# Performance work log

Measured on AMD Instinct MI355X. Metric: run time of the kernel, lower is better.

## Reference

```python
import jax, jax.numpy as jnp
import numpy as np

EPS = 1e-4
GX, GY, ZMAX = 512, 512, 64
S0 = (GX, GY, ZMAX)

# ---------- rulebook construction (numpy, setup-time only) ----------

def _lin(c, S):
    return (c[:, 0].astype(np.int64) * S[1] + c[:, 1]) * S[2] + c[:, 2]

def _lookup(skeys, order, qk):
    pos = np.searchsorted(skeys, qk)
    pc = np.clip(pos, 0, len(skeys) - 1)
    ok = skeys[pc] == qk
    return np.where(ok, order[pc], -1).astype(np.int32)

def _sm_rulebook(coords, S):
    # submanifold 3x3x3: for each active site, index of neighbor at each of 27 offsets (-1 if inactive)
    keys = _lin(coords, S)
    order = np.argsort(keys).astype(np.int64); skeys = keys[order]
    Sa = np.array(S)
    cols = []
    for d in [(i, j, k) for i in (-1, 0, 1) for j in (-1, 0, 1) for k in (-1, 0, 1)]:
        q = coords + np.array(d)
        inb = np.all((q >= 0) & (q < Sa), axis=1)
        nb = _lookup(skeys, order, _lin(np.clip(q, 0, None), S))
        cols.append(np.where(inb, nb, -1).astype(np.int32))
    return np.stack(cols, 1)  # [N, 27]

def _down_rulebook(coords, S):
    # strided 2x2x2 conv: coarse sites = unique(coords//2); [Nc, 8] child indices into fine level
    Sc = (S[0] // 2, S[1] // 2, S[2] // 2)
    pk = np.unique(_lin(coords // 2, Sc))
    z = pk % Sc[2]; y = (pk // Sc[2]) % Sc[1]; x = pk // (Sc[1] * Sc[2])
    pcoords = np.stack([x, y, z], 1)
    keys = _lin(coords, S)
    order = np.argsort(keys).astype(np.int64); skeys = keys[order]
    cols = []
    for d in [(i, j, k) for i in (0, 1) for j in (0, 1) for k in (0, 1)]:
        cols.append(_lookup(skeys, order, _lin(pcoords * 2 + np.array(d), S)))
    return np.stack(cols, 1), pcoords, Sc

def _coords0():
    # road-like 2.5D surface: one active voxel per (x, y) column -> exactly 512*512 unique sites
    xs, ys = np.meshgrid(np.arange(GX), np.arange(GY), indexing='ij')
    x = xs.ravel().astype(np.int64); y = ys.ravel().astype(np.int64)
    z = (32 + 8 * np.sin(x / 37.0) + 8 * np.cos(y / 53.0) + 3 * np.sin((x + y) / 17.0)).astype(np.int64)
    z = np.clip(z, 0, ZMAX - 1)
    return np.stack([x, y, z], 1)


def setup_inputs() -> dict:
    c0 = _coords0()
    nbr_0 = _sm_rulebook(c0, S0)
    rb_0, c1, S1 = _down_rulebook(c0, S0)
    nbr_1 = _sm_rulebook(c1, S1)
    rb_1, c2, S2 = _down_rulebook(c1, S1)
    nbr_2 = _sm_rulebook(c2, S2)

    key = jax.random.key(0)
    ks = iter(jax.random.split(key, 40))
    def w(shape):
        fan = float(np.prod(shape[:-1]))
        return (jax.random.normal(next(ks), shape, jnp.float32) / np.sqrt(fan)).astype(jnp.float32)
    def gb(c):  # row 0 = gamma (~1), row 1 = beta (~0)
        base = jnp.concatenate([jnp.ones((1, c), jnp.float32), jnp.zeros((1, c), jnp.float32)], 0)
        return base + 0.01 * jax.random.normal(next(ks), (2, c), jnp.float32)

    N0 = c0.shape[0]
    return dict(
        feat=jax.random.normal(next(ks), (N0, 3), jnp.float32),
        w_in=w((27, 3, 32)),
        bn1_0=gb(32), w_sm1_0=w((27, 32, 32)),
        bnd_0=gb(32), w_down_0=w((8, 32, 64)),
        bn1_1=gb(64), w_sm1_1=w((27, 64, 64)),
        bnd_1=gb(64), w_down_1=w((8, 64, 96)),
        bn1_2=gb(96), w_sm1_2=w((27, 96, 96)),
        bnu_1=gb(96), w_up_1=w((8, 96, 64)),
        bn2_1=gb(128), w_sm2_1=w((27, 128, 64)),
        bnu_0=gb(64), w_up_0=w((8, 64, 32)),
        bn2_0=gb(64), w_sm2_0=w((27, 64, 32)),
        bnf=gb(32),
        lin_w=w((32, 2)), lin_b=jnp.zeros((2,), jnp.float32),
        nbr_0=jnp.asarray(nbr_0), nbr_1=jnp.asarray(nbr_1), nbr_2=jnp.asarray(nbr_2),
        rb_0=jnp.asarray(rb_0), rb_1=jnp.asarray(rb_1),
    )

# ---------- jax forward ----------

def bn_relu(x, gb):
    # SCN BatchNormReLU: normalize over all active sites (biased var), affine, then ReLU
    mu = jnp.mean(x, 0)
    var = jnp.var(x, 0)
    return jax.nn.relu((x - mu) * (gb[0] / jnp.sqrt(var + EPS)) + gb[1])

def sm_conv(feat, nbr, W):
    # submanifold conv: gather 27 neighbors (zero for inactive), per-offset GEMM, accumulate
    out = jnp.zeros((feat.shape[0], W.shape[2]), feat.dtype)
    for k in range(W.shape[0]):
        idx = nbr[:, k]
        g = jnp.where((idx >= 0)[:, None], feat[jnp.clip(idx, 0)], 0.0)
        out = out + g @ W[k]
    return out

def down_conv(feat, rb, W):
    # strided 2x2x2 conv: gather children of each coarse site
    out = jnp.zeros((rb.shape[0], W.shape[2]), feat.dtype)
    for k in range(W.shape[0]):
        idx = rb[:, k]
        g = jnp.where((idx >= 0)[:, None], feat[jnp.clip(idx, 0)], 0.0)
        out = out + g @ W[k]
    return out

def up_conv(feat_c, rb, W, n_fine):
    # deconv (transpose of down_conv): scatter coarse features back to fine active sites
    out = jnp.zeros((n_fine, W.shape[2]), feat_c.dtype)
    for k in range(W.shape[0]):
        idx = rb[:, k]
        contrib = jnp.where((idx >= 0)[:, None], feat_c @ W[k], 0.0)
        out = out.at[jnp.clip(idx, 0)].add(contrib)
    return out


def reference(feat, w_in, bn1_0, w_sm1_0, bnd_0, w_down_0, bn1_1, w_sm1_1, bnd_1, w_down_1,
              bn1_2, w_sm1_2, bnu_1, w_up_1, bn2_1, w_sm2_1, bnu_0, w_up_0, bn2_0, w_sm2_0,
              bnf, lin_w, lin_b, nbr_0, nbr_1, nbr_2, rb_0, rb_1):
    x0 = sm_conv(feat, nbr_0, w_in)                              # initial SMConv 3 -> 32
    x0 = sm_conv(bn_relu(x0, bn1_0), nbr_0, w_sm1_0)             # level-0 entry block
    d0 = down_conv(bn_relu(x0, bnd_0), rb_0, w_down_0)           # [N1, 64]
    x1 = sm_conv(bn_relu(d0, bn1_1), nbr_1, w_sm1_1)             # level-1 entry block
    d1 = down_conv(bn_relu(x1, bnd_1), rb_1, w_down_1)           # [N2, 96]
    x2 = sm_conv(bn_relu(d1, bn1_2), nbr_2, w_sm1_2)             # innermost block
    u1 = up_conv(bn_relu(x2, bnu_1), rb_1, w_up_1, x1.shape[0])  # deconv 96 -> 64
    y1 = sm_conv(bn_relu(jnp.concatenate([x1, u1], 1), bn2_1), nbr_1, w_sm2_1)  # 128 -> 64
    u0 = up_conv(bn_relu(y1, bnu_0), rb_0, w_up_0, x0.shape[0])  # deconv 64 -> 32
    y0 = sm_conv(bn_relu(jnp.concatenate([x0, u0], 1), bn2_0), nbr_0, w_sm2_0)  # 64 -> 32
    out = bn_relu(y0, bnf)                                       # final BatchNormReLU(m)
    return out @ lin_w + lin_b                                   # Linear(m, 2)
```

## Files before the change

### kernel.cpp

```cpp
#include <hip/hip_runtime.h>
#include <hip/hip_bf16.h>


typedef __hip_bfloat16 hbf;
typedef __attribute__((ext_vector_type(8))) short short8;
typedef __attribute__((ext_vector_type(4))) float f32x4;
typedef const __attribute__((address_space(1))) short gas_short;
typedef __attribute__((address_space(3))) short las_short;

__device__ inline float b2f(short s) {
    unsigned u = ((unsigned)(unsigned short)s) << 16;
    float f; __builtin_memcpy(&f, &u, 4); return f;
}
__device__ inline short f2b(float f) {
    hbf h = __float2bfloat16(f);
    short s; __builtin_memcpy(&s, &h, 2); return s;
}

struct WPA {
    const float* src[9];
    short* dst[9];
    int CI[9], CO[9];
    int cum[10];
};
__global__ __launch_bounds__(256) void wprep_all(WPA a, int total) {
    int e0 = blockIdx.x * 256 + threadIdx.x;
    if (e0 >= total) return;
    int L = 0;
#pragma unroll
    for (int i = 1; i < 9; i++) L += (e0 >= a.cum[i]) ? 1 : 0;
    int e = e0 - a.cum[L];
    int CI = a.CI[L], CO = a.CO[L];
    int NT = CO >> 4, NCH = CI >> 5;
    int j    = e & 7;
    int lane = (e >> 3) & 63;
    int t    = (e >> 9) % NT;
    int c    = (e / (512 * NT)) % NCH;
    int k    = e / (512 * NT * NCH);
    int ci = c * 32 + (lane >> 4) * 8 + j;
    int co = t * 16 + (lane & 15);
    a.dst[L][e] = f2b(a.src[L][((long long)k * CI + ci) * CO + co]);
}

__global__ void zerok(float* p, int n) {
    int i = blockIdx.x * 256 + threadIdx.x;
    if (i < n) p[i] = 0.f;
}

__global__ __launch_bounds__(256) void nbrmask_k(const int* __restrict__ nbr,
                                                 unsigned* __restrict__ msk, int N) {
    long long r = (long long)blockIdx.x * 256 + threadIdx.x;
    if (r >= N) return;
    unsigned mv = 0;
#pragma unroll
    for (int k = 0; k < 27; k++)
        mv |= (nbr[r * 27 + k] >= 0) ? (1u << k) : 0u;
    msk[r] = mv;
}

__global__ __launch_bounds__(256) void conv_in_st(
    const float* __restrict__ feat, const unsigned* __restrict__ msk,
    const float* __restrict__ W, short* __restrict__ out, int N) {
    __shared__ float sW[27 * 96];
    __shared__ float sF[3][258][3];
    const int tid = threadIdx.x;
    const int bid = blockIdx.x;
    const int xq     = bid >> 1;
    const int ystart = (bid & 1) << 8;
    const long long R = (long long)bid * 256;

    for (int e = tid; e < 27 * 96; e += 256) sW[e] = W[e];
    for (int e = tid; e < 3 * 258; e += 256) {
        int rr = e % 258, st = e / 258;
        long long gr = (long long)(xq - 1 + st) * 512 + (ystart - 1 + rr);
        long long grc = (gr < 0 || gr >= N) ? 0 : gr;
        sF[st][rr][0] = feat[grc * 3];
        sF[st][rr][1] = feat[grc * 3 + 1];
        sF[st][rr][2] = feat[grc * 3 + 2];
    }
    __syncthreads();

    long long r = R + tid;
    unsigned mv = (r < N) ? msk[r] : 0u;
    float acc[32];
#pragma unroll
    for (int c = 0; c < 32; c++) acc[c] = 0.f;
#pragma unroll
    for (int k = 0; k < 27; k++) {
        if (mv & (1u << k)) {
            const int st = k / 9;
            const int dy = (k / 3) % 3 - 1;
            const int rl = 1 + tid + dy;
            float f0 = sF[st][rl][0];
            float f1 = sF[st][rl][1];
            float f2 = sF[st][rl][2];
            const float* w = sW + k * 96;
#pragma unroll
            for (int c = 0; c < 32; c++)
                acc[c] += f0 * w[c] + f1 * w[32 + c] + f2 * w[64 + c];
        }
    }
    if (r < N) {
#pragma unroll
        for (int c = 0; c < 32; c++) out[r * 32 + c] = f2b(acc[c]);
    }
}

template<int CI1, int CI2, int COUT>
__global__ __launch_bounds__(256) void stencil0(
    const short* __restrict__ fA, const short* __restrict__ fB,
    const unsigned* __restrict__ msk, const short* __restrict__ Wf,
    short* __restrict__ out, float* __restrict__ pstat,
    const float* __restrict__ abA, const float* __restrict__ abB, int N) {
    constexpr int CIT  = CI1 + CI2;
    constexpr int NCH  = CIT / 32;
    constexpr int NT   = COUT / 16;
    constexpr int MT   = 2;
    constexpr int CIB  = CIT * 2;
    constexpr int ROWS = 130;
    constexpr int NC8  = CIT / 8;
    constexpr int SWB  = (CIB >= 128) ? 7 : 3;
    __shared__ __attribute__((aligned(16))) char sA[3 * ROWS * CIB];
    const int tid  = threadIdx.x;
    const int lane = tid & 63;
    const int wid  = tid >> 6;
    const int m    = lane & 15;
    const int quad = lane >> 4;
    const int bid  = blockIdx.x;
    const int xq     = bid >> 2;
    const int ystart = (bid & 3) << 7;
    const long long R = (long long)bid * 128;

    {
        const int c8 = tid % NC8;
        const bool isA = (c8 * 8) < CI1;
        const short* src  = isA ? fA : fB;
        const float* abp  = isA ? abA : abB;
        const int   srcCI = isA ? CI1 : CI2;
        const int   chb   = isA ? c8 * 8 : c8 * 8 - CI1;
        float s_[8], b_[8];
#pragma unroll
        for (int jj = 0; jj < 8; jj++) {
            s_[jj] = abp[chb + jj];
            b_[jj] = abp[srcCI + chb + jj];
        }
        for (int e = tid; e < 3 * ROWS * NC8; e += 256) {
            int rr = (e / NC8) % ROWS;
            int st = e / (NC8 * ROWS);
            long long gr = (long long)(xq - 1 + st) * 512 + (ystart - 1 + rr);
            long long grc = (gr < 0 || gr >= N) ? 0 : gr;
            short8 v = *reinterpret_cast<const short8*>(src + grc * srcCI + chb);
            short8 o;
#pragma unroll
            for (int jj = 0; jj < 8; jj++) {
                float f = b2f(v[jj]) * s_[jj] + b_[jj];
                o[jj] = f2b(f > 0.f ? f : 0.f);
            }
            int byte = (st * ROWS + rr) * CIB + c8 * 16;
            byte ^= ((rr & SWB) << 4);
            *reinterpret_cast<short8*>(sA + byte) = o;
        }
    }
    __syncthreads();

    f32x4 acc[MT][NT];
#pragma unroll
    for (int mt = 0; mt < MT; mt++)
#pragma unroll
        for (int t = 0; t < NT; t++) acc[mt][t] = (f32x4)0.f;

    unsigned mv[MT];
#pragma unroll
    for (int mt = 0; mt < MT; mt++) {
        long long r = R + wid * 32 + mt * 16 + m;
        mv[mt] = (r < N) ? msk[r] : 0u;
    }

#pragma unroll
    for (int s9 = 0; s9 < 9; s9++) {
        const int st = s9 / 3;
        const int dy = s9 % 3 - 1;
        short8 a[MT][NCH];
#pragma unroll
        for (int mt = 0; mt < MT; mt++) {
            int rl = 1 + wid * 32 + mt * 16 + m + dy;
#pragma unroll
            for (int c = 0; c < NCH; c++) {
                int byte = (st * ROWS + rl) * CIB + (c * 4 + quad) * 16;
                byte ^= ((rl & SWB) << 4);
                a[mt][c] = *reinterpret_cast<const short8*>(sA + byte);
            }
        }
#pragma unroll
        for (int z3 = 0; z3 < 3; z3++) {
            const int k = s9 * 3 + z3;
            unsigned anyb = (mv[0] >> k) & 1;
            if (MT > 1) anyb |= (mv[1] >> k) & 1;
            if (__any(anyb)) {
                short8 bf[NCH][NT];
#pragma unroll
                for (int c = 0; c < NCH; c++)
#pragma unroll
                    for (int t = 0; t < NT; t++)
                        bf[c][t] = *reinterpret_cast<const short8*>(
                            Wf + ((size_t)(k * NCH + c) * NT + t) * 512 + lane * 8);
#pragma unroll
                for (int mt = 0; mt < MT; mt++) {
                    const bool bb = (mv[mt] >> k) & 1;
                    short8 asel[NCH];
#pragma unroll
                    for (int c = 0; c < NCH; c++)
                        asel[c] = bb ? a[mt][c] : (short8)0;
#pragma unroll
                    for (int c = 0; c < NCH; c++)
#pragma unroll
                        for (int t = 0; t < NT; t++)
                            acc[mt][t] = __builtin_amdgcn_mfma_f32_16x16x32_bf16(
                                asel[c], bf[c][t], acc[mt][t], 0, 0, 0);
                }
            }
        }
    }

    float s[NT], q[NT];
#pragma unroll
    for (int t = 0; t < NT; t++) { s[t] = 0.f; q[t] = 0.f; }
#pragma unroll
    for (int mt = 0; mt < MT; mt++) {
#pragma unroll
        for (int g4 = 0; g4 < 4; g4++) {
            long long sr = R + wid * 32 + mt * 16 + quad * 4 + g4;
            if (sr < N) {
#pragma unroll
                for (int t = 0; t < NT; t++) {
                    float v = acc[mt][t][g4];
                    out[sr * COUT + t * 16 + m] = f2b(v);
                    s[t] += v; q[t] += v * v;
                }
            }
        }
    }
    float* pb = pstat + (blockIdx.x & 7) * 2 * COUT;
#pragma unroll
    for (int t = 0; t < NT; t++) {
        float sv = s[t], qv = q[t];
        sv += __shfl_xor(sv, 16); qv += __shfl_xor(qv, 16);
        sv += __shfl_xor(sv, 32); qv += __shfl_xor(qv, 32);
        if (quad == 0) {
            atomicAdd(&pb[t * 16 + m], sv);
            atomicAdd(&pb[COUT + t * 16 + m], qv);
        }
    }
}

template<int CI1, int CI2, int COUT, int K, int G, int MT, bool FACT>
__global__ __launch_bounds__(256) void gmfma10(
    const short* __restrict__ fA, const short* __restrict__ fB,
    const int* __restrict__ nbr, const short* __restrict__ Wf,
    short* __restrict__ out, float* __restrict__ pstat,
    const float* __restrict__ abp, int N) {
    static_assert(K % G == 0, "G must divide K");
    static_assert(!FACT || CI2 == 0, "fused act only for single input");
    constexpr int NT  = COUT / 16;
    constexpr int NC1 = CI1 / 32;
    constexpr int NC2 = CI2 / 32;
    constexpr int NCH = (CI1 + CI2) / 32;
    constexpr int PANEL = NCH * NT * 512;
    constexpr int GSH   = G * PANEL;
    constexpr int NPH   = K / G;
    constexpr int WCH   = GSH / 4;
    constexpr int S16   = (WCH * 2) / 1024;
    constexpr int S4    = ((WCH * 2) % 1024) / 256;
    __shared__ __attribute__((aligned(16))) short sB[GSH];
    const int tid  = threadIdx.x;
    const int lane = tid & 63;
    const int wid  = tid >> 6;
    const int m    = lane & 15;
    const int quad = lane >> 4;
    const long long tb0 = ((long long)blockIdx.x * 4 + wid) * (MT * 16);

    f32x4 acc[MT][NT];
#pragma unroll
    for (int mt = 0; mt < MT; mt++)
#pragma unroll
        for (int t = 0; t < NT; t++) acc[mt][t] = (f32x4)0.f;

#define STAGE(ph)                                                              \
    {                                                                          \
        const short* _src = Wf + (size_t)(ph) * GSH + wid * WCH;               \
        short* _dst = &sB[wid * WCH];                                          \
        _Pragma("unroll")                                                      \
        for (int i = 0; i < S16; i++)                                          \
            __builtin_amdgcn_global_load_lds(                                  \
                (gas_short*)(_src + i * 512 + lane * 8),                       \
                (las_short*)(_dst + i * 512), 16, 0, 0);                       \
        _Pragma("unroll")                                                      \
        for (int i = 0; i < S4; i++)                                           \
            __builtin_amdgcn_global_load_lds(                                  \
                (gas_short*)(_src + S16 * 512 + i * 128 + lane * 2),           \
                (las_short*)(_dst + S16 * 512 + i * 128), 4, 0, 0);            \
    }

    STAGE(0)
    __builtin_amdgcn_sched_barrier(0);

    int idxs[MT][K];
#pragma unroll
    for (int mt = 0; mt < MT; mt++) {
        long long r = tb0 + mt * 16 + m;
        bool rv = r < N;
#pragma unroll
        for (int k = 0; k < K; k++)
            idxs[mt][k] = rv ? nbr[r * K + k] : -1;
    }
    unsigned pmask[MT];
#pragma unroll
    for (int mt = 0; mt < MT; mt++) {
        unsigned pm = 0;
#pragma unroll
        for (int k = 0; k < K; k++)
            pm |= __any(idxs[mt][k] >= 0) ? (1u << k) : 0u;
        pmask[mt] = __builtin_amdgcn_readfirstlane(pm);
    }

    float aS[FACT ? NC1 * 8 : 1], aBb[FACT ? NC1 * 8 : 1];
    if constexpr (FACT) {
#pragma unroll
        for (int c = 0; c < NC1; c++)
#pragma unroll
            for (int jj = 0; jj < 8; jj++) {
                int ch = c * 32 + quad * 8 + jj;
                aS[c * 8 + jj]  = abp[ch];
                aBb[c * 8 + jj] = abp[CI1 + ch];
            }
    }

    __builtin_amdgcn_sched_barrier(0);
    asm volatile("s_waitcnt vmcnt(0)" ::: "memory");
    __builtin_amdgcn_s_barrier();
    __builtin_amdgcn_sched_barrier(0);
    asm volatile("" ::: "memory");

    short8 S[3][NCH];

#define LOADS(sl, mt, kk)                                                      \
    {                                                                          \
        int _i = idxs[mt][kk];                                                 \
        long long _j = _i < 0 ? 0 : _i;                                        \
        _Pragma("unroll")                                                      \
        for (int c = 0; c < NC1; c++) {                                        \
            short8 _v = *reinterpret_cast<const short8*>(                      \
                fA + _j * CI1 + c * 32 + quad * 8);                            \
            if constexpr (FACT) {                                              \
                short8 _o;                                                     \
                _Pragma("unroll")                                              \
                for (int jj = 0; jj < 8; jj++) {                               \
                    float _f = b2f(_v[jj]) * aS[c * 8 + jj] + aBb[c * 8 + jj]; \
                    _o[jj] = f2b(_f > 0.f ? _f : 0.f);                         \
                }                                                              \
                _v = _o;                                                       \
            }                                                                  \
            S[sl][c] = (_i >= 0) ? _v : (short8)0;                             \
        }                                                                      \
        if constexpr (NC2 > 0) {                                               \
            _Pragma("unroll")                                                  \
            for (int c = 0; c < NC2; c++) {                                    \
                short8 _v = *reinterpret_cast<const short8*>(                  \
                    fB + _j * CI2 + c * 32 + quad * 8);                        \
                S[sl][NC1 + c] = (_i >= 0) ? _v : (short8)0;                   \
            }                                                                  \
        }                                                                      \
    }
#define MFMAS(sl, mt, jl)                                                      \
    {                                                                          \
        _Pragma("unroll")                                                      \
        for (int c = 0; c < NCH; c++) {                                        \
            _Pragma("unroll")                                                  \
            for (int t = 0; t < NT; t++) {                                     \
                short8 b = *reinterpret_cast<const short8*>(                   \
                    &sB[((jl) * NCH * NT + c * NT + t) * 512 + lane * 8]);     \
                acc[mt][t] = __builtin_amdgcn_mfma_f32_16x16x32_bf16(          \
                    S[sl][c], b, acc[mt][t], 0, 0, 0);                         \
            }                                                                  \
        }                                                                      \
    }

#pragma unroll
    for (int ph = 0; ph < NPH; ph++) {
#pragma unroll
        for (int mt = 0; mt < MT; mt++) {
            const unsigned mm = (pmask[mt] >> (ph * G)) & ((1u << G) - 1);
#pragma unroll
            for (int j = 0; j < G + 2; j++) {
                if (j < G)
                    if (mm & (1u << j)) LOADS(j % 3, mt, ph * G + j)
                if (j >= 2)
                    if (mm & (1u << (j - 2))) MFMAS((j - 2) % 3, mt, j - 2)
            }
        }
        if (ph + 1 < NPH) {
            __builtin_amdgcn_sched_barrier(0);
            asm volatile("s_waitcnt lgkmcnt(0)" ::: "memory");
            __builtin_amdgcn_s_barrier();
            __builtin_amdgcn_sched_barrier(0);
            STAGE(ph + 1)
            __builtin_amdgcn_sched_barrier(0);
            asm volatile("s_waitcnt vmcnt(0)" ::: "memory");
            __builtin_amdgcn_s_barrier();
            __builtin_amdgcn_sched_barrier(0);
            asm volatile("" ::: "memory");
        }
    }
#undef LOADS
#undef MFMAS
#undef STAGE
    float s[NT], q[NT];
#pragma unroll
    for (int t = 0; t < NT; t++) { s[t] = 0.f; q[t] = 0.f; }
#pragma unroll
    for (int mt = 0; mt < MT; mt++) {
#pragma unroll
        for (int g4 = 0; g4 < 4; g4++) {
            long long sr = tb0 + mt * 16 + quad * 4 + g4;
            if (sr < N) {
#pragma unroll
                for (int t = 0; t < NT; t++) {
                    float v = acc[mt][t][g4];
                    out[sr * COUT + t * 16 + m] = f2b(v);
                    s[t] += v; q[t] += v * v;
                }
            }
        }
    }
    float* pb = pstat + (blockIdx.x & 7) * 2 * COUT;
#pragma unroll
    for (int t = 0; t < NT; t++) {
        float sv = s[t], qv = q[t];
        sv += __shfl_xor(sv, 16); qv += __shfl_xor(qv, 16);
        sv += __shfl_xor(sv, 32); qv += __shfl_xor(qv, 32);
        if (quad == 0) {
            atomicAdd(&pb[t * 16 + m], sv);
            atomicAdd(&pb[COUT + t * 16 + m], qv);
        }
    }
}

template<int CIN, int COUT, int G>
__global__ __launch_bounds__(256) void upmfma10(
    const short* __restrict__ f, const int* __restrict__ rb,
    const short* __restrict__ Wf, short* __restrict__ out,
    float* __restrict__ pstat, const float* __restrict__ abp, int N) {
    static_assert(8 % G == 0, "G must divide 8");
    constexpr int NT = COUT / 16;
    constexpr int NK = CIN / 32;
    constexpr int PANEL = NK * NT * 512;
    constexpr int GSH   = G * PANEL;
    constexpr int NPH   = 8 / G;
    constexpr int WCH   = GSH / 4;
    constexpr int S16   = (WCH * 2) / 1024;
    constexpr int S4    = ((WCH * 2) % 1024) / 256;
    __shared__ __attribute__((aligned(16))) short sB[GSH];
    const int tid  = threadIdx.x;
    const int lane = tid & 63;
    const int wid  = tid >> 6;
    const int m    = lane & 15;
    const int quad = lane >> 4;
    const long long row0 = ((long long)blockIdx.x * 4 + wid) * 16;
    const long long r = row0 + m;
    const bool rv = r < N;
    const long long rc = rv ? r : 0;

#define STAGE(ph)                                                              \
    {                                                                          \
        const short* _src = Wf + (size_t)(ph) * GSH + wid * WCH;               \
        short* _dst = &sB[wid * WCH];                                          \
        _Pragma("unroll")                                                      \
        for (int i = 0; i < S16; i++)                                          \
            __builtin_amdgcn_global_load_lds(                                  \
                (gas_short*)(_src + i * 512 + lane * 8),                       \
                (las_short*)(_dst + i * 512), 16, 0, 0);                       \
        _Pragma("unroll")                                                      \
        for (int i = 0; i < S4; i++)                                           \
            __builtin_amdgcn_global_load_lds(                                  \
                (gas_short*)(_src + S16 * 512 + i * 128 + lane * 2),           \
                (las_short*)(_dst + S16 * 512 + i * 128), 4, 0, 0);            \
    }
    STAGE(0)
    __builtin_amdgcn_sched_barrier(0);

    short8 af[NK];
#pragma unroll
    for (int kc = 0; kc < NK; kc++) {
        short8 v = *reinterpret_cast<const short8*>(
            f + rc * CIN + kc * 32 + quad * 8);
        short8 o;
#pragma unroll
        for (int jj = 0; jj < 8; jj++) {
            int ch = kc * 32 + quad * 8 + jj;
            float u = b2f(v[jj]) * abp[ch] + abp[CIN + ch];
            o[jj] = f2b(u > 0.f ? u : 0.f);
        }
        af[kc] = rv ? o : (short8)0;
    }
    int sidx[8][4];
#pragma unroll
    for (int g4 = 0; g4 < 4; g4++) {
        long long sr = row0 + quad * 4 + g4;
#pragma unroll
        for (int k = 0; k < 8; k++)
            sidx[k][g4] = (sr < N) ? rb[sr * 8 + k] : -1;
    }
    unsigned pm = 0;
#pragma unroll
    for (int k = 0; k < 8; k++) {
        int anyv = (sidx[k][0] >= 0) | (sidx[k][1] >= 0) |
                   (sidx[k][2] >= 0) | (sidx[k][3] >= 0);
        pm |= __any(anyv) ? (1u << k) : 0u;
    }
    pm = __builtin_amdgcn_readfirstlane(pm);

    float s[NT], q[NT];
#pragma unroll
    for (int t = 0; t < NT; t++) { s[t] = 0.f; q[t] = 0.f; }

    __builtin_amdgcn_sched_barrier(0);
    asm volatile("s_waitcnt vmcnt(0)" ::: "memory");
    __builtin_amdgcn_s_barrier();
    __builtin_amdgcn_sched_barrier(0);
    asm volatile("" ::: "memory");

#pragma unroll
    for (int ph = 0; ph < NPH; ph++) {
#pragma unroll
        for (int j = 0; j < G; j++) {
            const int k = ph * G + j;
            if (pm & (1u << k)) {
                f32x4 acc[NT];
#pragma unroll
                for (int t = 0; t < NT; t++) acc[t] = (f32x4)0.f;
#pragma unroll
                for (int kc = 0; kc < NK; kc++) {
#pragma unroll
                    for (int t = 0; t < NT; t++) {
                        short8 b = *reinterpret_cast<const short8*>(
                            &sB[(j * NK * NT + kc * NT + t) * 512 + lane * 8]);
                        acc[t] = __builtin_amdgcn_mfma_f32_16x16x32_bf16(
                            af[kc], b, acc[t], 0, 0, 0);
                    }
                }
#pragma unroll
                for (int g4 = 0; g4 < 4; g4++) {
                    if (sidx[k][g4] >= 0) {
#pragma unroll
                        for (int t = 0; t < NT; t++) {
                            float v = acc[t][g4];
                            out[(long long)sidx[k][g4] * COUT + t * 16 + m] =
                                f2b(v);
                            s[t] += v; q[t] += v * v;
                        }
                    }
                }
            }
        }
        if (ph + 1 < NPH) {
            __builtin_amdgcn_sched_barrier(0);
            asm volatile("s_waitcnt lgkmcnt(0)" ::: "memory");
            __builtin_amdgcn_s_barrier();
            __builtin_amdgcn_sched_barrier(0);
            STAGE(ph + 1)
            __builtin_amdgcn_sched_barrier(0);
            asm volatile("s_waitcnt vmcnt(0)" ::: "memory");
            __builtin_amdgcn_s_barrier();
            __builtin_amdgcn_sched_barrier(0);
            asm volatile("" ::: "memory");
        }
    }
#undef STAGE
    float* pb = pstat + (blockIdx.x & 7) * 2 * COUT;
#pragma unroll
    for (int t = 0; t < NT; t++) {
        float sv = s[t], qv = q[t];
        sv += __shfl_xor(sv, 16); qv += __shfl_xor(qv, 16);
        sv += __shfl_xor(sv, 32); qv += __shfl_xor(qv, 32);
        if (quad == 0) {
            atomicAdd(&pb[t * 16 + m], sv);
            atomicAdd(&pb[COUT + t * 16 + m], qv);
        }
    }
}

template<int C>
__global__ void bn_stats(const short* __restrict__ x, double* __restrict__ part, int N) {
    constexpr int GR  = C / 8;
    constexpr int RPB = 256 / GR;
    constexpr int ACTIVE = GR * RPB;
    __shared__ double ls[256 * 8];
    __shared__ double lq[256 * 8];
    const int tid = threadIdx.x;
    const int g   = tid % GR;
    const int rr  = tid / GR;
    double s[8], q[8];
#pragma unroll
    for (int j = 0; j < 8; j++) { s[j] = 0.0; q[j] = 0.0; }
    if (tid < ACTIVE) {
        for (long long r = (long long)blockIdx.x * RPB + rr; r < N;
             r += (long long)gridDim.x * RPB) {
            short8 v = *reinterpret_cast<const short8*>(x + r * C + g * 8);
#pragma unroll
            for (int j = 0; j < 8; j++) {
                double f = (double)b2f(v[j]);
                s[j] += f; q[j] += f * f;
            }
        }
    }
#pragma unroll
    for (int j = 0; j < 8; j++) { ls[tid * 8 + j] = s[j]; lq[tid * 8 + j] = q[j]; }
    __syncthreads();
    if (tid < C) {
        int gg = tid / 8, jj = tid % 8;
        double S = 0.0, Q = 0.0;
        for (int r2 = 0; r2 < RPB; r2++) {
            S += ls[(r2 * GR + gg) * 8 + jj];
            Q += lq[(r2 * GR + gg) * 8 + jj];
        }
        part[blockIdx.x * 256 + tid]       = S;
        part[blockIdx.x * 256 + 128 + tid] = Q;
    }
}

__global__ void bn_fin(const double* __restrict__ part, const float* __restrict__ gb,
                       int gbfull, int goff, float* __restrict__ ab,
                       int C, int P, double invN) {
    __shared__ double ss[256], sq[256];
    const int tid = threadIdx.x;
    const int c   = tid % C;
    const int g   = tid / C;
    const int G   = 256 / C;
    double s = 0.0, q = 0.0;
    if (g < G) {
        for (int p = g; p < P; p += G) {
            s += part[p * 256 + c];
            q += part[p * 256 + 128 + c];
        }
    }
    ss[tid] = s; sq[tid] = q;
    __syncthreads();
    if (tid < C) {
        for (int j = 1; j < G; j++) { s += ss[j * C + c]; q += sq[j * C + c]; }
        double mu  = s * invN;
        double var = q * invN - mu * mu;
        double a   = (double)gb[goff + c] / sqrt(var + 1e-4);
        ab[c]     = (float)a;
        ab[C + c] = (float)((double)gb[gbfull + goff + c] - mu * a);
    }
}

__global__ void bn_fin_a(const float* __restrict__ pst, const float* __restrict__ gb,
                         int gbfull, int goff, float* __restrict__ ab,
                         int C, double invN) {
    int c = threadIdx.x;
    if (c >= C) return;
    double s = 0.0, q = 0.0;
#pragma unroll
    for (int b = 0; b < 8; b++) {
        s += (double)pst[b * 2 * C + c];
        q += (double)pst[b * 2 * C + C + c];
    }
    double mu  = s * invN;
    double var = q * invN - mu * mu;
    double a   = (double)gb[goff + c] / sqrt(var + 1e-4);
    ab[c]     = (float)a;
    ab[C + c] = (float)((double)gb[gbfull + goff + c] - mu * a);
}

template<int C>
__global__ void bnact(const short* __restrict__ x, const float* __restrict__ ab,
                      short* __restrict__ y, long long total8) {
    long long i = (long long)blockIdx.x * blockDim.x + threadIdx.x;
    if (i >= total8) return;
    long long base = i * 8;
    int c0 = (int)(base % C);
    short8 v = *reinterpret_cast<const short8*>(x + base);
    short8 o;
#pragma unroll
    for (int j = 0; j < 8; j++) {
        float f = b2f(v[j]) * ab[c0 + j] + ab[C + c0 + j];
        o[j] = f2b(f > 0.f ? f : 0.f);
    }
    *reinterpret_cast<short8*>(y + base) = o;
}

template<int C>
__global__ void bnact2(const short* __restrict__ xa, const float* __restrict__ aba,
                       short* __restrict__ ya,
                       const short* __restrict__ xb, const float* __restrict__ abb,
                       short* __restrict__ yb, long long n8) {
    long long i = (long long)blockIdx.x * blockDim.x + threadIdx.x;
    if (i >= 2 * n8) return;
    const short* x; const float* ab; short* y; long long ii;
    if (i < n8) { x = xa; ab = aba; y = ya; ii = i; }
    else        { x = xb; ab = abb; y = yb; ii = i - n8; }
    long long base = ii * 8;
    int c0 = (int)(base % C);
    short8 v = *reinterpret_cast<const short8*>(x + base);
    short8 o;
#pragma unroll
    for (int j = 0; j < 8; j++) {
        float f = b2f(v[j]) * ab[c0 + j] + ab[C + c0 + j];
        o[j] = f2b(f > 0.f ? f : 0.f);
    }
    *reinterpret_cast<short8*>(y + base) = o;
}

__global__ void final_k(const short* __restrict__ x, const float* __restrict__ ab,
                        const float* __restrict__ lw, const float* __restrict__ lb,
                        float* __restrict__ out, int N) {
    long long r = (long long)blockIdx.x * blockDim.x + threadIdx.x;
    if (r >= N) return;
    float a0 = lb[0], a1 = lb[1];
#pragma unroll
    for (int j = 0; j < 4; j++) {
        short8 v = *reinterpret_cast<const short8*>(x + r * 32 + j * 8);
#pragma unroll
        for (int t = 0; t < 8; t++) {
            int ci = 8 * j + t;
            float u = b2f(v[t]) * ab[ci] + ab[32 + ci];
            u = u > 0.f ? u : 0.f;
            a0 += u * lw[ci * 2];
            a1 += u * lw[ci * 2 + 1];
        }
    }
    out[2 * r]     = a0;
    out[2 * r + 1] = a1;
}

extern "C" void kernel_launch(void* const* d_in, const int* in_sizes, int n_in,
                              void* d_out, int out_size, void* d_ws, size_t ws_size,
                              hipStream_t stream) {
    const long long N0 = in_sizes[0] / 3;
    const long long N1 = in_sizes[26] / 8;
    const long long N2 = in_sizes[27] / 8;
    const int P = 256;

    const float* feat = (const float*)d_in[0];
    const int* nbr0 = (const int*)d_in[23];
    const int* nbr1 = (const int*)d_in[24];
    const int* nbr2 = (const int*)d_in[25];
    const int* rb0  = (const int*)d_in[26];
    const int* rb1  = (const int*)d_in[27];

    char* p = (char*)d_ws;
    double* part = (double*)p;            p += (size_t)P * 256 * 8;
    float*  ab   = (float*)p;             p += 12 * 256 * 4;
    float*  pst  = (float*)p;             p += (size_t)10 * 2048 * 4;
    unsigned* msk0 = (unsigned*)p;        p += ((size_t)N0 * 4 + 63) & ~(size_t)63;
    const int wLayer[9] = {3, 5, 7, 9, 11, 13, 15, 17, 19};
    const int wK[9]  = {27, 8, 27, 8, 27, 8, 27, 8, 27};
    const int wCI[9] = {32, 32, 64, 64, 96, 96, 128, 64, 64};
    const int wCO[9] = {32, 64, 64, 96, 96, 64, 64, 32, 32};
    short* wt[9];
    WPA wpa;
    int cum = 0;
    for (int i = 0; i < 9; i++) {
        wt[i] = (short*)p;
        int n = wK[i] * wCI[i] * wCO[i];
        p += (((size_t)n * 2 + 63) & ~(size_t)63);
        wpa.src[i] = (const float*)d_in[wLayer[i]];
        wpa.dst[i] = wt[i];
        wpa.CI[i] = wCI[i]; wpa.CO[i] = wCO[i];
        wpa.cum[i] = cum; cum += n;
    }
    wpa.cum[9] = cum;
    auto balloc = [&](long long elems) {
        short* q = (short*)p;
        p += (((size_t)elems * 2 + 63) & ~(size_t)63);
        return q;
    };
    short* R0 = balloc(N0 * 32);
    short* R1 = balloc(N0 * 32);
    short* R2 = balloc(N1 * 64);
    short* R3 = balloc(N0 * 32);
    short* Xb = balloc(N0 * 32);
    short* Yb = balloc(N0 * 32);

    wprep_all<<<(cum + 255) / 256, 256, 0, stream>>>(wpa, cum);
    zerok<<<(10 * 2048 + 255) / 256, 256, 0, stream>>>(pst, 10 * 2048);
    nbrmask_k<<<(int)((N0 + 255) / 256), 256, 0, stream>>>(nbr0, msk0, (int)N0);

#define AB(SL) (ab + (SL) * 256)
#define PS(SL) (pst + (SL) * 2048)
#define FINA(PSL, GBI, GBFULL, GOFF, SL, CH, NN)                                     \
    bn_fin_a<<<1, 128, 0, stream>>>(PS(PSL), (const float*)d_in[GBI], GBFULL, GOFF,  \
                                    AB(SL), CH, 1.0 / (double)(NN))
#define GB1(N_) (int)(((N_) + 63) / 64)
#define GB2(N_) (int)(((N_) + 127) / 128)

    conv_in_st<<<(int)((N0 + 255) / 256), 256, 0, stream>>>(
        feat, msk0, (const float*)d_in[1], R0, (int)N0);
    bn_stats<32><<<P, 256, 0, stream>>>(R0, part, (int)N0);
    bn_fin<<<1, 256, 0, stream>>>(part, (const float*)d_in[2], 32, 0,
                                  AB(0), 32, P, 1.0 / (double)N0);
    stencil0<32, 0, 32><<<GB2(N0), 256, 0, stream>>>(
        R0, nullptr, msk0, wt[0], R1, PS(0), AB(0), nullptr, (int)N0);
    FINA(0, 4, 32, 0, 1, 32, N0);
    FINA(0, 18, 64, 0, 9, 32, N0);
    gmfma10<32, 0, 64, 8, 8, 2, true><<<GB2(N1), 256, 0, stream>>>(
        R1, nullptr, rb0, wt[1], R0, PS(1), AB(1), (int)N1);
    FINA(1, 6, 64, 0, 2, 64, N1);

    bnact<64><<<(int)((N1 * 64 / 8 + 255) / 256), 256, 0, stream>>>(
        R0, AB(2), Xb, N1 * 64 / 8);
    gmfma10<64, 0, 64, 27, 3, 2, false><<<GB2(N1), 256, 0, stream>>>(
        Xb, nullptr, nbr1, wt[2], R2, PS(2), nullptr, (int)N1);
    FINA(2, 8, 64, 0, 3, 64, N1);
    FINA(2, 14, 128, 0, 6, 64, N1);
    gmfma10<64, 0, 96, 8, 2, 1, true><<<GB1(N2), 256, 0, stream>>>(
        R2, nullptr, rb1, wt[3], R0, PS(3), AB(3), (int)N2);
    FINA(3, 10, 96, 0, 4, 96, N2);

    bnact<96><<<(int)((N2 * 96 / 8 + 255) / 256), 256, 0, stream>>>(
        R0, AB(4), Xb, N2 * 96 / 8);
    gmfma10<96, 0, 96, 27, 3, 1, false><<<GB1(N2), 256, 0, stream>>>(
        Xb, nullptr, nbr2, wt[4], R3, PS(4), nullptr, (int)N2);
    FINA(4, 12, 96, 0, 5, 96, N2);

    upmfma10<96, 64, 2><<<GB1(N2), 256, 0, stream>>>(
        R3, rb1, wt[5], R0, PS(5), AB(5), (int)N2);
    FINA(5, 14, 128, 64, 7, 64, N1);
    bnact2<64><<<(int)((2 * (N1 * 64 / 8) + 255) / 256), 256, 0, stream>>>(
        R2, AB(6), Xb, R0, AB(7), Yb, N1 * 64 / 8);
    gmfma10<64, 64, 64, 27, 3, 2, false><<<GB2(N1), 256, 0, stream>>>(
        Xb, Yb, nbr1, wt[6], R3, PS(6), nullptr, (int)N1);
    FINA(6, 16, 64, 0, 8, 64, N1);

    upmfma10<64, 32, 4><<<GB1(N1), 256, 0, stream>>>(
        R3, rb0, wt[7], R0, PS(7), AB(8), (int)N1);
    FINA(7, 18, 64, 32, 10, 32, N0);
    stencil0<32, 32, 32><<<GB2(N0), 256, 0, stream>>>(
        R1, R0, msk0, wt[8], R3, PS(8), AB(9), AB(10), (int)N0);
    FINA(8, 20, 32, 0, 11, 32, N0);

    final_k<<<(int)((N0 + 255) / 256), 256, 0, stream>>>(
        R3, AB(11), (const float*)d_in[21], (const float*)d_in[22],
        (float*)d_out, (int)N0);

#undef AB
#undef PS
#undef FINA
#undef GB1
#undef GB2
}
```

Measured before the change: 556.8 us.

## Fold BN finalize into consumer kernel prologues and merge stat zeroing

Removes the eleven single-block bn_fin_a launches. Each consumer kernel now reduces the partial statistics itself in its prologue and writes the BN scale and bias to shared memory. The zeroing of the statistics buffer moves into the neighbor-mask kernel, which drops one more launch. In exchange every block recomputes the same small double-precision reduction and adds a block-wide barrier, and the zeroing relies on the mask kernel launching at least 20480 threads.

```diff
diff --git a/kernel.cpp b/kernel.cpp
--- a/kernel.cpp
+++ b/kernel.cpp
@@ -15,6 +15,34 @@
 __device__ inline short f2b(float f) {
     hbf h = __float2bfloat16(f);
     short s; __builtin_memcpy(&s, &h, 2); return s;
+}
+
+struct BNP {
+    const float* pst;
+    const float* abd;
+    const float* gb;
+    int gbfull, goff;
+    double invN;
+};
+__device__ inline void bn_load(const BNP& p, int C, float* lab, int tid) {
+    if (tid < C) {
+        if (p.pst) {
+            double s = 0.0, q = 0.0;
+#pragma unroll
+            for (int b = 0; b < 8; b++) {
+                s += (double)p.pst[b * 2 * C + tid];
+                q += (double)p.pst[b * 2 * C + C + tid];
+            }
+            double mu  = s * p.invN;
+            double var = q * p.invN - mu * mu;
+            double a   = (double)p.gb[p.goff + tid] / sqrt(var + 1e-4);
+            lab[tid]     = (float)a;
+            lab[C + tid] = (float)((double)p.gb[p.gbfull + p.goff + tid] - mu * a);
+        } else {
+            lab[tid]     = p.abd[tid];
+            lab[C + tid] = p.abd[C + tid];
+        }
+    }
 }
 
 struct WPA {
@@ -42,14 +70,11 @@
     a.dst[L][e] = f2b(a.src[L][((long long)k * CI + ci) * CO + co]);
 }
 
-__global__ void zerok(float* p, int n) {
-    int i = blockIdx.x * 256 + threadIdx.x;
-    if (i < n) p[i] = 0.f;
-}
-
 __global__ __launch_bounds__(256) void nbrmask_k(const int* __restrict__ nbr,
-                                                 unsigned* __restrict__ msk, int N) {
+                                                 unsigned* __restrict__ msk,
+                                                 float* __restrict__ pst, int N) {
     long long r = (long long)blockIdx.x * 256 + threadIdx.x;
+    if (r < 10 * 2048) pst[r] = 0.f;
     if (r >= N) return;
     unsigned mv = 0;
 #pragma unroll
@@ -111,7 +136,7 @@
     const short* __restrict__ fA, const short* __restrict__ fB,
     const unsigned* __restrict__ msk, const short* __restrict__ Wf,
     short* __restrict__ out, float* __restrict__ pstat,
-    const float* __restrict__ abA, const float* __restrict__ abB, int N) {
+    BNP pA, BNP pB, int N) {
     constexpr int CIT  = CI1 + CI2;
     constexpr int NCH  = CIT / 32;
     constexpr int NT   = COUT / 16;
@@ -121,6 +146,8 @@
     constexpr int NC8  = CIT / 8;
     constexpr int SWB  = (CIB >= 128) ? 7 : 3;
     __shared__ __attribute__((aligned(16))) char sA[3 * ROWS * CIB];
+    __shared__ float labA[2 * CI1];
+    __shared__ float labB[CI2 > 0 ? 2 * CI2 : 1];
     const int tid  = threadIdx.x;
     const int lane = tid & 63;
     const int wid  = tid >> 6;
@@ -131,18 +158,22 @@
     const int ystart = (bid & 3) << 7;
     const long long R = (long long)bid * 128;
 
+    bn_load(pA, CI1, labA, tid);
+    if constexpr (CI2 > 0) bn_load(pB, CI2, labB, tid);
+    __syncthreads();
+
     {
         const int c8 = tid % NC8;
         const bool isA = (c8 * 8) < CI1;
         const short* src  = isA ? fA : fB;
-        const float* abp  = isA ? abA : abB;
+        const float* lab  = isA ? labA : labB;
         const int   srcCI = isA ? CI1 : CI2;
         const int   chb   = isA ? c8 * 8 : c8 * 8 - CI1;
         float s_[8], b_[8];
 #pragma unroll
         for (int jj = 0; jj < 8; jj++) {
-            s_[jj] = abp[chb + jj];
-            b_[jj] = abp[srcCI + chb + jj];
+            s_[jj] = lab[chb + jj];
+            b_[jj] = lab[srcCI + chb + jj];
         }
         for (int e = tid; e < 3 * ROWS * NC8; e += 256) {
             int rr = (e / NC8) % ROWS;
@@ -257,8 +288,7 @@
 __global__ __launch_bounds__(256) void gmfma10(
     const short* __restrict__ fA, const short* __restrict__ fB,
     const int* __restrict__ nbr, const short* __restrict__ Wf,
-    short* __restrict__ out, float* __restrict__ pstat,
-    const float* __restrict__ abp, int N) {
+    short* __restrict__ out, float* __restrict__ pstat, BNP pF, int N) {
     static_assert(K % G == 0, "G must divide K");
     static_assert(!FACT || CI2 == 0, "fused act only for single input");
     constexpr int NT  = COUT / 16;
@@ -272,6 +302,7 @@
     constexpr int S16   = (WCH * 2) / 1024;
     constexpr int S4    = ((WCH * 2) % 1024) / 256;
     __shared__ __attribute__((aligned(16))) short sB[GSH];
+    __shared__ float labF[FACT ? 2 * CI1 : 1];
     const int tid  = threadIdx.x;
     const int lane = tid & 63;
     const int wid  = tid >> 6;
@@ -284,6 +315,20 @@
     for (int mt = 0; mt < MT; mt++)
 #pragma unroll
         for (int t = 0; t < NT; t++) acc[mt][t] = (f32x4)0.f;
+
+    float aS[FACT ? NC1 * 8 : 1], aBb[FACT ? NC1 * 8 : 1];
+    if constexpr (FACT) {
+        bn_load(pF, CI1, labF, tid);
+        __syncthreads();
+#pragma unroll
+        for (int c = 0; c < NC1; c++)
+#pragma unroll
+            for (int jj = 0; jj < 8; jj++) {
+                int ch = c * 32 + quad * 8 + jj;
+                aS[c * 8 + jj]  = labF[ch];
+                aBb[c * 8 + jj] = labF[CI1 + ch];
+            }
+    }
 
 #define STAGE(ph)                                                              \
     {                                                                          \
@@ -321,18 +366,6 @@
         for (int k = 0; k < K; k++)
             pm |= __any(idxs[mt][k] >= 0) ? (1u << k) : 0u;
         pmask[mt] = __builtin_amdgcn_readfirstlane(pm);
-    }
-
-    float aS[FACT ? NC1 * 8 : 1], aBb[FACT ? NC1 * 8 : 1];
-    if constexpr (FACT) {
-#pragma unroll
-        for (int c = 0; c < NC1; c++)
-#pragma unroll
-            for (int jj = 0; jj < 8; jj++) {
-                int ch = c * 32 + quad * 8 + jj;
-                aS[c * 8 + jj]  = abp[ch];
-                aBb[c * 8 + jj] = abp[CI1 + ch];
-            }
     }
 
     __builtin_amdgcn_sched_barrier(0);
@@ -449,7 +482,7 @@
 __global__ __launch_bounds__(256) void upmfma10(
     const short* __restrict__ f, const int* __restrict__ rb,
     const short* __restrict__ Wf, short* __restrict__ out,
-    float* __restrict__ pstat, const float* __restrict__ abp, int N) {
+    float* __restrict__ pstat, BNP pF, int N) {
     static_assert(8 % G == 0, "G must divide 8");
     constexpr int NT = COUT / 16;
     constexpr int NK = CIN / 32;
@@ -460,6 +493,7 @@
     constexpr int S16   = (WCH * 2) / 1024;
     constexpr int S4    = ((WCH * 2) % 1024) / 256;
     __shared__ __attribute__((aligned(16))) short sB[GSH];
+    __shared__ float labF[2 * CIN];
     const int tid  = threadIdx.x;
     const int lane = tid & 63;
     const int wid  = tid >> 6;
@@ -469,6 +503,9 @@
     const long long r = row0 + m;
     const bool rv = r < N;
     const long long rc = rv ? r : 0;
+
+    bn_load(pF, CIN, labF, tid);
+    __syncthreads();
 
 #define STAGE(ph)                                                              \
     {                                                                          \
@@ -497,7 +534,7 @@
 #pragma unroll
         for (int jj = 0; jj < 8; jj++) {
             int ch = kc * 32 + quad * 8 + jj;
-            float u = b2f(v[jj]) * abp[ch] + abp[CIN + ch];
+            float u = b2f(v[jj]) * labF[ch] + labF[CIN + ch];
             o[jj] = f2b(u > 0.f ? u : 0.f);
         }
         af[kc] = rv ? o : (short8)0;
@@ -655,28 +692,14 @@
     }
 }
 
-__global__ void bn_fin_a(const float* __restrict__ pst, const float* __restrict__ gb,
-                         int gbfull, int goff, float* __restrict__ ab,
-                         int C, double invN) {
-    int c = threadIdx.x;
-    if (c >= C) return;
-    double s = 0.0, q = 0.0;
-#pragma unroll
-    for (int b = 0; b < 8; b++) {
-        s += (double)pst[b * 2 * C + c];
-        q += (double)pst[b * 2 * C + C + c];
-    }
-    double mu  = s * invN;
-    double var = q * invN - mu * mu;
-    double a   = (double)gb[goff + c] / sqrt(var + 1e-4);
-    ab[c]     = (float)a;
-    ab[C + c] = (float)((double)gb[gbfull + goff + c] - mu * a);
-}
-
 template<int C>
-__global__ void bnact(const short* __restrict__ x, const float* __restrict__ ab,
-                      short* __restrict__ y, long long total8) {
-    long long i = (long long)blockIdx.x * blockDim.x + threadIdx.x;
+__global__ __launch_bounds__(256) void bnact_i(
+    const short* __restrict__ x, BNP p, short* __restrict__ y, long long total8) {
+    __shared__ float lab[2 * C];
+    const int tid = threadIdx.x;
+    bn_load(p, C, lab, tid);
+    __syncthreads();
+    long long i = (long long)blockIdx.x * 256 + tid;
     if (i >= total8) return;
     long long base = i * 8;
     int c0 = (int)(base % C);
@@ -684,38 +707,47 @@
     short8 o;
 #pragma unroll
     for (int j = 0; j < 8; j++) {
-        float f = b2f(v[j]) * ab[c0 + j] + ab[C + c0 + j];
+        float f = b2f(v[j]) * lab[c0 + j] + lab[C + c0 + j];
         o[j] = f2b(f > 0.f ? f : 0.f);
     }
     *reinterpret_cast<short8*>(y + base) = o;
 }
 
 template<int C>
-__global__ void bnact2(const short* __restrict__ xa, const float* __restrict__ aba,
-                       short* __restrict__ ya,
-                       const short* __restrict__ xb, const float* __restrict__ abb,
-                       short* __restrict__ yb, long long n8) {
-    long long i = (long long)blockIdx.x * blockDim.x + threadIdx.x;
+__global__ __launch_bounds__(256) void bnact2_i(
+    const short* __restrict__ xa, BNP pa, short* __restrict__ ya,
+    const short* __restrict__ xb, BNP pb, short* __restrict__ yb, long long n8) {
+    __shared__ float la[2 * C], lb[2 * C];
+    const int tid = threadIdx.x;
+    bn_load(pa, C, la, tid);
+    bn_load(pb, C, lb, tid);
+    __syncthreads();
+    long long i = (long long)blockIdx.x * 256 + tid;
     if (i >= 2 * n8) return;
-    const short* x; const float* ab; short* y; long long ii;
-    if (i < n8) { x = xa; ab = aba; y = ya; ii = i; }
-    else        { x = xb; ab = abb; y = yb; ii = i - n8; }
+    const short* x; const float* lab; short* y; long long ii;
+    if (i < n8) { x = xa; lab = la; y = ya; ii = i; }
+    else        { x = xb; lab = lb; y = yb; ii = i - n8; }
     long long base = ii * 8;
     int c0 = (int)(base % C);
     short8 v = *reinterpret_cast<const short8*>(x + base);
     short8 o;
 #pragma unroll
     for (int j = 0; j < 8; j++) {
-        float f = b2f(v[j]) * ab[c0 + j] + ab[C + c0 + j];
+        float f = b2f(v[j]) * lab[c0 + j] + lab[C + c0 + j];
         o[j] = f2b(f > 0.f ? f : 0.f);
     }
     *reinterpret_cast<short8*>(y + base) = o;
 }
 
-__global__ void final_k(const short* __restrict__ x, const float* __restrict__ ab,
-                        const float* __restrict__ lw, const float* __restrict__ lb,
-                        float* __restrict__ out, int N) {
-    long long r = (long long)blockIdx.x * blockDim.x + threadIdx.x;
+__global__ __launch_bounds__(256) void final_k_i(
+    const short* __restrict__ x, BNP p,
+    const float* __restrict__ lw, const float* __restrict__ lb,
+    float* __restrict__ out, int N) {
+    __shared__ float lab[64];
+    const int tid = threadIdx.x;
+    bn_load(p, 32, lab, tid);
+    __syncthreads();
+    long long r = (long long)blockIdx.x * 256 + tid;
     if (r >= N) return;
     float a0 = lb[0], a1 = lb[1];
 #pragma unroll
@@ -724,7 +756,7 @@
 #pragma unroll
         for (int t = 0; t < 8; t++) {
             int ci = 8 * j + t;
-            float u = b2f(v[t]) * ab[ci] + ab[32 + ci];
+            float u = b2f(v[t]) * lab[ci] + lab[32 + ci];
             u = u > 0.f ? u : 0.f;
             a0 += u * lw[ci * 2];
             a1 += u * lw[ci * 2 + 1];
@@ -784,16 +816,22 @@
     short* Yb = balloc(N0 * 32);
 
     wprep_all<<<(cum + 255) / 256, 256, 0, stream>>>(wpa, cum);
-    zerok<<<(10 * 2048 + 255) / 256, 256, 0, stream>>>(pst, 10 * 2048);
-    nbrmask_k<<<(int)((N0 + 255) / 256), 256, 0, stream>>>(nbr0, msk0, (int)N0);
+    nbrmask_k<<<(int)((N0 + 255) / 256), 256, 0, stream>>>(nbr0, msk0, pst, (int)N0);
 
 #define AB(SL) (ab + (SL) * 256)
 #define PS(SL) (pst + (SL) * 2048)
-#define FINA(PSL, GBI, GBFULL, GOFF, SL, CH, NN)                                     \
-    bn_fin_a<<<1, 128, 0, stream>>>(PS(PSL), (const float*)d_in[GBI], GBFULL, GOFF,  \
-                                    AB(SL), CH, 1.0 / (double)(NN))
 #define GB1(N_) (int)(((N_) + 63) / 64)
 #define GB2(N_) (int)(((N_) + 127) / 128)
+
+    auto mkp = [&](float* pstp, const float* abd, int gbi, int gbfull, int goff,
+                   double invN) {
+        BNP b;
+        b.pst = pstp; b.abd = abd;
+        b.gb = (gbi >= 0) ? (const float*)d_in[gbi] : nullptr;
+        b.gbfull = gbfull; b.goff = goff; b.invN = invN;
+        return b;
+    };
+    BNP dummy = mkp(nullptr, nullptr, -1, 0, 0, 0.0);
 
     conv_in_st<<<(int)((N0 + 255) / 256), 256, 0, stream>>>(
         feat, msk0, (const float*)d_in[1], R0, (int)N0);
@@ -801,52 +839,49 @@
     bn_fin<<<1, 256, 0, stream>>>(part, (const float*)d_in[2], 32, 0,
                                   AB(0), 32, P, 1.0 / (double)N0);
     stencil0<32, 0, 32><<<GB2(N0), 256, 0, stream>>>(
-        R0, nullptr, msk0, wt[0], R1, PS(0), AB(0), nullptr, (int)N0);
-    FINA(0, 4, 32, 0, 1, 32, N0);
-    FINA(0, 18, 64, 0, 9, 32, N0);
+        R0, nullptr, msk0, wt[0], R1, PS(0),
+        mkp(nullptr, AB(0), -1, 0, 0, 0.0), dummy, (int)N0);
     gmfma10<32, 0, 64, 8, 8, 2, true><<<GB2(N1), 256, 0, stream>>>(
-        R1, nullptr, rb0, wt[1], R0, PS(1), AB(1), (int)N1);
-    FINA(1, 6, 64, 0, 2, 64, N1);
-
-    bnact<64><<<(int)((N1 * 64 / 8 + 255) / 256), 256, 0, stream>>>(
-        R0, AB(2), Xb, N1 * 64 / 8);
+        R1, nullptr, rb0, wt[1], R0, PS(1),
+        mkp(PS(0), nullptr, 4, 32, 0, 1.0 / (double)N0), (int)N1);
+
+    bnact_i<64><<<(int)((N1 * 64 / 8 + 255) / 256), 256, 0, stream>>>(
+        R0, mkp(PS(1), nullptr, 6, 64, 0, 1.0 / (double)N1), Xb, N1 * 64 / 8);
     gmfma10<64, 0, 64, 27, 3, 2, false><<<GB2(N1), 256, 0, stream>>>(
-        Xb, nullptr, nbr1, wt[2], R2, PS(2), nullptr, (int)N1);
-    FINA(2, 8, 64, 0, 3, 64, N1);
-    FINA(2, 14, 128, 0, 6, 64, N1);
+        Xb, nullptr, nbr1, wt[2], R2, PS(2), dummy, (int)N1);
     gmfma10<64, 0, 96, 8, 2, 1, true><<<GB1(N2), 256, 0, stream>>>(
-        R2, nullptr, rb1, wt[3], R0, PS(3), AB(3), (int)N2);
-    FINA(3, 10, 96, 0, 4, 96, N2);
-
-    bnact<96><<<(int)((N2 * 96 / 8 + 255) / 256), 256, 0, stream>>>(
-        R0, AB(4), Xb, N2 * 96 / 8);
+        R2, nullptr, rb1, wt[3], R0, PS(3),
+        mkp(PS(2), nullptr, 8, 64, 0, 1.0 / (double)N1), (int)N2);
+
+    bnact_i<96><<<(int)((N2 * 96 / 8 + 255) / 256), 256, 0, stream>>>(
+        R0, mkp(PS(3), nullptr, 10, 96, 0, 1.0 / (double)N2), Xb, N2 * 96 / 8);
     gmfma10<96, 0, 96, 27, 3, 1, false><<<GB1(N2), 256, 0, stream>>>(
-        Xb, nullptr, nbr2, wt[4], R3, PS(4), nullptr, (int)N2);
-    FINA(4, 12, 96, 0, 5, 96, N2);
+        Xb, nullptr, nbr2, wt[4], R3, PS(4), dummy, (int)N2);
 
     upmfma10<96, 64, 2><<<GB1(N2), 256, 0, stream>>>(
-        R3, rb1, wt[5], R0, PS(5), AB(5), (int)N2);
-    FINA(5, 14, 128, 64, 7, 64, N1);
-    bnact2<64><<<(int)((2 * (N1 * 64 / 8) + 255) / 256), 256, 0, stream>>>(
-        R2, AB(6), Xb, R0, AB(7), Yb, N1 * 64 / 8);
+        R3, rb1, wt[5], R0, PS(5),
+        mkp(PS(4), nullptr, 12, 96, 0, 1.0 / (double)N2), (int)N2);
+    bnact2_i<64><<<(int)((2 * (N1 * 64 / 8) + 255) / 256), 256, 0, stream>>>(
+        R2, mkp(PS(2), nullptr, 14, 128, 0, 1.0 / (double)N1), Xb,
+        R0, mkp(PS(5), nullptr, 14, 128, 64, 1.0 / (double)N1), Yb, N1 * 64 / 8);
     gmfma10<64, 64, 64, 27, 3, 2, false><<<GB2(N1), 256, 0, stream>>>(
-        Xb, Yb, nbr1, wt[6], R3, PS(6), nullptr, (int)N1);
-    FINA(6, 16, 64, 0, 8, 64, N1);
+        Xb, Yb, nbr1, wt[6], R3, PS(6), dummy, (int)N1);
 
     upmfma10<64, 32, 4><<<GB1(N1), 256, 0, stream>>>(
-        R3, rb0, wt[7], R0, PS(7), AB(8), (int)N1);
-    FINA(7, 18, 64, 32, 10, 32, N0);
+        R3, rb0, wt[7], R0, PS(7),
+        mkp(PS(6), nullptr, 16, 64, 0, 1.0 / (double)N1), (int)N1);
     stencil0<32, 32, 32><<<GB2(N0), 256, 0, stream>>>(
-        R1, R0, msk0, wt[8], R3, PS(8), AB(9), AB(10), (int)N0);
-    FINA(8, 20, 32, 0, 11, 32, N0);
-
-    final_k<<<(int)((N0 + 255) / 256), 256, 0, stream>>>(
-        R3, AB(11), (const float*)d_in[21], (const float*)d_in[22],
+        R1, R0, msk0, wt[8], R3, PS(8),
+        mkp(PS(0), nullptr, 18, 64, 0, 1.0 / (double)N0),
+        mkp(PS(7), nullptr, 18, 64, 32, 1.0 / (double)N0), (int)N0);
+
+    final_k_i<<<(int)((N0 + 255) / 256), 256, 0, stream>>>(
+        R3, mkp(PS(8), nullptr, 20, 32, 0, 1.0 / (double)N0),
+        (const float*)d_in[21], (const float*)d_in[22],
         (float*)d_out, (int)N0);
 
 #undef AB
 #undef PS
-#undef FINA
 #undef GB1
 #undef GB2
 }
```

Measured after the change: 536.6 us. 3.6% less time.
